# Performance work log

Hardware: AMD Instinct MI355X
Metric: run time of the kernel (lower is better)

The kernel has to match this reference:

```python
import jax, jax.numpy as jnp
import numpy as np

B, N, D_IN, D_OUT, L, T = 8, 512, 1024, 1024, 16, 4096


def setup_inputs() -> dict:
    key = jax.random.key(0)
    k1, k2, k3 = jax.random.split(key, 3)
    pooled_vectors = jax.random.normal(k1, (B, N, D_IN), dtype=jnp.float32)
    # stacked nn.Linear weights, each (out, in), bias=False
    W = jax.random.normal(k2, (L, D_OUT, D_IN), dtype=jnp.float32) * 0.02
    pooling_indices = jnp.sort(jax.random.randint(k3, (N,), 0, T, dtype=jnp.int64))
    return {
        "pooled_vectors": pooled_vectors,
        "W": W,
        "pooling_indices": pooling_indices,
        "target_length": T,
    }


def reference(pooled_vectors, W, pooling_indices, target_length):
    # pooled_vectors: (B, N, D_in); W: (L, D_out, D_in); pooling_indices: (N,) sorted
    Bn, Nn, _ = pooled_vectors.shape
    Ln = W.shape[0]
    t = jnp.arange(target_length)
    # segment i covers [start_i, idx_i + 1); searchsorted finds the covering segment
    seg = jnp.searchsorted(pooling_indices, t, side="left")  # (T,)
    valid = seg < Nn  # positions past the last pooling index stay zero
    segc = jnp.clip(seg, 0, Nn - 1)
    start = jnp.where(segc > 0, pooling_indices[segc - 1] + 1, 0)
    lidx = jnp.minimum(t - start, Ln - 1)  # position-specific linear index, capped
    # apply all L position linears to every pooled vector: (B, N, L, D_out)
    trans = jnp.einsum("bnd,lod->bnlo", pooled_vectors, W)
    out = trans[:, segc, lidx]  # gather per output position -> (B, T, D_out)
    return jnp.where(valid[None, :, None], out, jnp.zeros((), out.dtype))
```

## Files before the change

### kernel.cpp

```cpp
#include <hip/hip_runtime.h>
#include <stdint.h>

#define B_    8
#define N_    512
#define DIN   1024
#define DOUT  1024
#define L_    16
#define T_    4096

#define BM 256
#define BN 128
#define BK 32
#define NB (DOUT / BN)
#define NKT (DIN / BK)
#define MT_MAX 160
#define ZROW ((long)B_ * N_)

typedef __attribute__((ext_vector_type(8))) short short8;
typedef __attribute__((ext_vector_type(4))) float f32x4;

#define POOLED_ELEMS ((long)B_ * N_ * DIN + DIN)
#define WS_W_OFF     ((size_t)POOLED_ELEMS * 2)
#define WS_META_OFF  (WS_W_OFF + (size_t)L_ * DOUT * DIN * 2)

__device__ __forceinline__ unsigned short f2bf(float f) {
  unsigned u = __float_as_uint(f);
  u += 0x7FFFu + ((u >> 16) & 1u);
  return (unsigned short)(u >> 16);
}

__device__ __forceinline__ void gload_lds16(const void* g, void* l) {
  __builtin_amdgcn_global_load_lds(
      (const __attribute__((address_space(1))) void*)g,
      (__attribute__((address_space(3))) void*)l, 16, 0, 0);
}

__device__ __forceinline__ void bar() {
  asm volatile("" ::: "memory");
  __builtin_amdgcn_s_barrier();
  asm volatile("" ::: "memory");
}

__global__ void k_convert(const float* __restrict__ pooled,
                          const float* __restrict__ W,
                          unsigned short* __restrict__ wsP,
                          unsigned short* __restrict__ wsW) {
  const long np4 = (long)B_ * N_ * DIN / 4;
  const long nw4 = (long)L_ * DOUT * DIN / 4;
  const long nz4 = DIN / 4;
  long i = (long)blockIdx.x * blockDim.x + threadIdx.x;
  const long stride = (long)gridDim.x * blockDim.x;
  for (; i < np4 + nw4 + nz4; i += stride) {
    if (i < np4) {
      float4 v = ((const float4*)pooled)[i];
      ushort4 o = { f2bf(v.x), f2bf(v.y), f2bf(v.z), f2bf(v.w) };
      ((ushort4*)wsP)[i] = o;
    } else if (i < np4 + nw4) {
      float4 v = ((const float4*)W)[i - np4];
      ushort4 o = { f2bf(v.x), f2bf(v.y), f2bf(v.z), f2bf(v.w) };
      ((ushort4*)wsW)[i - np4] = o;
    } else {
      ushort4 z = {0, 0, 0, 0};
      ((ushort4*)wsP)[i - nw4] = z;
    }
  }
}

__global__ void k_prep(const int* __restrict__ pidx,
                       unsigned* __restrict__ tlist,
                       int* __restrict__ goff, int* __restrict__ grows,
                       unsigned* __restrict__ table, int* __restrict__ ntiles) {
  __shared__ int sp[N_];
  __shared__ unsigned smap[T_];
  __shared__ int cnt[L_], pos[L_];
  const int tid = threadIdx.x;
  for (int i = tid; i < N_; i += 256) sp[i] = pidx[i];
  if (tid < L_) cnt[tid] = 0;
  __syncthreads();
  for (int t = tid; t < T_; t += 256) {
    int lo = 0, hi = N_;
    while (lo < hi) { int mid = (lo + hi) >> 1; if (sp[mid] < t) lo = mid + 1; else hi = mid; }
    int n, l;
    if (lo < N_) {
      int start = lo ? sp[lo - 1] + 1 : 0;
      int li = t - start;
      l = li > (L_ - 1) ? (L_ - 1) : li;
      n = lo;
    } else { n = 0xFFFF; l = L_ - 1; }
    smap[t] = (unsigned)n | ((unsigned)l << 16);
    atomicAdd(&cnt[l], 1);
  }
  __syncthreads();
  if (tid == 0) {
    int off = 0;
    for (int l = 0; l < L_; ++l) {
      pos[l] = off; goff[l] = off; grows[l] = cnt[l] * B_;
      off += cnt[l];
    }
  }
  __syncthreads();
  for (int t = tid; t < T_; t += 256) {
    unsigned m = smap[t];
    int l = m >> 16;
    int p = atomicAdd(&pos[l], 1);
    tlist[p] = (unsigned)t | ((m & 0xFFFFu) << 16);
  }
  __syncthreads();
  if (tid == 0) {
    int tt = 0;
    for (int l = 0; l < L_; ++l) {
      int rows = cnt[l] * B_;
      for (int r0 = 0; r0 < rows; r0 += BM) table[tt++] = (unsigned)l | ((unsigned)r0 << 4);
    }
    *ntiles = tt;
  }
}

__global__ __launch_bounds__(512, 4)
void k_gemm(const unsigned short* __restrict__ wsP,
            const unsigned short* __restrict__ wsW,
            const unsigned* __restrict__ tlist,
            const int* __restrict__ goff,
            const int* __restrict__ grows,
            const unsigned* __restrict__ table,
            const int* __restrict__ ntiles,
            float* __restrict__ out) {
  const int bid = blockIdx.x;
  const int mt = bid >> 3;
  const int nt = bid & 7;
  if (mt >= *ntiles) return;

  const unsigned te = table[mt];
  const int l    = te & 15;
  const int row0 = (int)(te >> 4);
  const int toff = goff[l];
  const int rows = grows[l];

  __shared__ __align__(16) unsigned short As[3][BM * BK];
  __shared__ __align__(16) unsigned short Bs[3][BN * BK];

  const int tid  = threadIdx.x;
  const int lane = tid & 63;
  const int w    = tid >> 6;
  const int wm   = w >> 1;
  const int wn   = w & 1;

  const int srow = tid >> 2;
  const int sx4  = ((tid & 3) ^ (srow & 3)) * 16;
  const char* aptr0;
  const char* aptr1;
  {
    long re[2];
#pragma unroll
    for (int r = 0; r < 2; ++r) {
      int rg = row0 + r * 128 + srow;
      if (rg < rows) {
        unsigned e = tlist[toff + (rg >> 3)];
        unsigned n = e >> 16;
        int b = rg & 7;
        re[r] = (n == 0xFFFFu) ? ZROW * (long)DIN
                               : ((long)(b * N_ + (int)n)) * DIN;
      } else re[r] = ZROW * (long)DIN;
    }
    aptr0 = (const char*)(wsP + re[0]) + sx4;
    aptr1 = (const char*)(wsP + re[1]) + sx4;
  }
  const char* bptr = (const char*)(wsW + ((long)l * DOUT + nt * BN + srow) * DIN) + sx4;

#define STG(t_, sb) do { \
  gload_lds16(aptr0 + (t_) * 64, (char*)As[sb] + w * 1024); \
  gload_lds16(aptr1 + (t_) * 64, (char*)As[sb] + 8192 + w * 1024); \
  gload_lds16(bptr  + (t_) * 64, (char*)Bs[sb] + w * 1024); } while (0)

  const int arow = wm * 64 + (lane & 15);
  const int brow = wn * 64 + (lane & 15);
  const int axr  = ((lane >> 4) ^ (lane & 3)) * 16;

  f32x4 acc[4][4];
#pragma unroll
  for (int m = 0; m < 4; ++m)
#pragma unroll
    for (int n = 0; n < 4; ++n)
      acc[m][n] = (f32x4){0.f, 0.f, 0.f, 0.f};

  short8 af[4], bf[4];

#define PHASE(t_, bb, sb) do { \
  const int t2_ = (t_) + 2; \
  if (t2_ < NKT) STG(t2_, sb); \
  _Pragma("unroll") for (int m_ = 0; m_ < 4; ++m_) \
    af[m_] = *(const short8*)((const char*)As[bb] + (arow + m_ * 16) * 64 + axr); \
  _Pragma("unroll") for (int n_ = 0; n_ < 4; ++n_) \
    bf[n_] = *(const short8*)((const char*)Bs[bb] + (brow + n_ * 16) * 64 + axr); \
  bar(); \
  asm volatile("s_waitcnt lgkmcnt(0)" ::: "memory"); \
  __builtin_amdgcn_s_setprio(1); \
  _Pragma("unroll") for (int n_ = 0; n_ < 4; ++n_) \
    _Pragma("unroll") for (int m_ = 0; m_ < 4; ++m_) \
      acc[m_][n_] = __builtin_amdgcn_mfma_f32_16x16x32_bf16(af[m_], bf[n_], acc[m_][n_], 0, 0, 0); \
  __builtin_amdgcn_s_setprio(0); \
  if (t2_ < NKT) asm volatile("s_waitcnt vmcnt(3)" ::: "memory"); \
  else           asm volatile("s_waitcnt vmcnt(0)" ::: "memory"); \
  bar(); \
} while (0)

  STG(0, 0);
  STG(1, 1);
  asm volatile("s_waitcnt vmcnt(3)" ::: "memory");
  bar();

  for (int j = 0; j < 11; ++j) {
    const int t0 = 3 * j;
    if (t0     < NKT) PHASE(t0,     0, 2);
    if (t0 + 1 < NKT) PHASE(t0 + 1, 1, 0);
    if (t0 + 2 < NKT) PHASE(t0 + 2, 2, 1);
  }

#pragma unroll
  for (int m = 0; m < 4; ++m) {
#pragma unroll
    for (int jj = 0; jj < 4; ++jj) {
      int rt = wm * 64 + m * 16 + (lane >> 4) * 4 + jj;
      int rg = row0 + rt;
      if (rg >= rows) continue;
      unsigned e = tlist[toff + (rg >> 3)];
      int b = rg & 7;
      int tt = (int)(e & 0xFFFFu);
      float* orow = out + ((long)b * T_ + tt) * DOUT + nt * BN + wn * 64 + (lane & 15);
#pragma unroll
      for (int n = 0; n < 4; ++n)
        orow[n * 16] = acc[m][n][jj];
    }
  }
#undef STG
#undef PHASE
}

extern "C" void kernel_launch(void* const* d_in, const int* in_sizes, int n_in,
                              void* d_out, int out_size, void* d_ws, size_t ws_size,
                              hipStream_t stream) {
  const float* pooled = (const float*)d_in[0];
  const float* W      = (const float*)d_in[1];
  const int*   pidx   = (const int*)d_in[2];
  float* out = (float*)d_out;

  char* ws = (char*)d_ws;
  unsigned short* wsP = (unsigned short*)(ws);
  unsigned short* wsW = (unsigned short*)(ws + WS_W_OFF);
  int* meta  = (int*)(ws + WS_META_OFF);
  unsigned* tlist = (unsigned*)meta;
  int* goff  = meta + T_;
  int* grows = meta + T_ + 16;
  unsigned* table = (unsigned*)(meta + T_ + 32);
  int* ntiles = meta + T_ + 32 + MT_MAX;

  k_prep<<<1, 256, 0, stream>>>(pidx, tlist, goff, grows, table, ntiles);
  k_convert<<<2048, 256, 0, stream>>>(pooled, W, wsP, wsW);
  k_gemm<<<MT_MAX * NB, 512, 0, stream>>>(wsP, wsW, tlist, goff, grows, table,
                                          ntiles, out);
}
```

Measured before the change: 141.8 us.

## Deduplicate capped-index output rows and change LDS swizzle pattern

The prep kernel now walks segments instead of positions. All positions within a segment that share the capped linear index L-1, and all positions past the last pooling index, are merged into one GEMM row carrying a repeat count of up to 255. The GEMM epilogue writes each result row to consecutive output positions. This cuts the number of GEMM rows in the last group (and the zero rows) at the cost of a serial store loop in the epilogue. The LDS XOR swizzle also changes to use bits 1-2 of the row, meant to reduce bank conflicts.

```diff
diff --git a/kernel.cpp b/kernel.cpp
--- a/kernel.cpp
+++ b/kernel.cpp
@@ -71,46 +71,62 @@
                        int* __restrict__ goff, int* __restrict__ grows,
                        unsigned* __restrict__ table, int* __restrict__ ntiles) {
   __shared__ int sp[N_];
-  __shared__ unsigned smap[T_];
   __shared__ int cnt[L_], pos[L_];
   const int tid = threadIdx.x;
-  for (int i = tid; i < N_; i += 256) sp[i] = pidx[i];
+  if (tid < N_) sp[tid] = pidx[tid];
   if (tid < L_) cnt[tid] = 0;
   __syncthreads();
-  for (int t = tid; t < T_; t += 256) {
-    int lo = 0, hi = N_;
-    while (lo < hi) { int mid = (lo + hi) >> 1; if (sp[mid] < t) lo = mid + 1; else hi = mid; }
-    int n, l;
-    if (lo < N_) {
-      int start = lo ? sp[lo - 1] + 1 : 0;
-      int li = t - start;
-      l = li > (L_ - 1) ? (L_ - 1) : li;
-      n = lo;
-    } else { n = 0xFFFF; l = L_ - 1; }
-    smap[t] = (unsigned)n | ((unsigned)l << 16);
-    atomicAdd(&cnt[l], 1);
+
+  int start = tid ? sp[tid - 1] + 1 : 0;
+  int len = sp[tid] - start + 1;
+  if (len < 0) len = 0;
+  const int nfull = len < 15 ? len : 15;
+
+  for (int l2 = 0; l2 < nfull; ++l2) atomicAdd(&cnt[l2], 1);
+  if (len > 15) atomicAdd(&cnt[15], (len - 15 + 254) / 255);
+  if (tid == N_ - 1) {
+    int invlen = T_ - 1 - sp[N_ - 1];
+    if (invlen > 0) atomicAdd(&cnt[15], (invlen + 254) / 255);
   }
   __syncthreads();
   if (tid == 0) {
     int off = 0;
-    for (int l = 0; l < L_; ++l) {
-      pos[l] = off; goff[l] = off; grows[l] = cnt[l] * B_;
-      off += cnt[l];
-    }
-  }
-  __syncthreads();
-  for (int t = tid; t < T_; t += 256) {
-    unsigned m = smap[t];
-    int l = m >> 16;
-    int p = atomicAdd(&pos[l], 1);
-    tlist[p] = (unsigned)t | ((m & 0xFFFFu) << 16);
+    for (int l2 = 0; l2 < L_; ++l2) {
+      pos[l2] = off; goff[l2] = off; grows[l2] = cnt[l2] * B_;
+      off += cnt[l2];
+    }
+  }
+  __syncthreads();
+
+  for (int l2 = 0; l2 < nfull; ++l2) {
+    int p = atomicAdd(&pos[l2], 1);
+    tlist[p] = (unsigned)(start + l2) | ((unsigned)tid << 12) | (1u << 22);
+  }
+  if (len > 15) {
+    int rem = len - 15, tt2 = start + 15;
+    while (rem > 0) {
+      int rr = rem > 255 ? 255 : rem;
+      int p = atomicAdd(&pos[15], 1);
+      tlist[p] = (unsigned)tt2 | ((unsigned)tid << 12) | ((unsigned)rr << 22);
+      tt2 += rr; rem -= rr;
+    }
+  }
+  if (tid == N_ - 1) {
+    int tt2 = sp[N_ - 1] + 1;
+    int rem = T_ - tt2;
+    while (rem > 0) {
+      int rr = rem > 255 ? 255 : rem;
+      int p = atomicAdd(&pos[15], 1);
+      tlist[p] = (unsigned)tt2 | (1023u << 12) | ((unsigned)rr << 22);
+      tt2 += rr; rem -= rr;
+    }
   }
   __syncthreads();
   if (tid == 0) {
     int tt = 0;
-    for (int l = 0; l < L_; ++l) {
-      int rows = cnt[l] * B_;
-      for (int r0 = 0; r0 < rows; r0 += BM) table[tt++] = (unsigned)l | ((unsigned)r0 << 4);
+    for (int l2 = 0; l2 < L_; ++l2) {
+      int rows = cnt[l2] * B_;
+      for (int r0 = 0; r0 < rows; r0 += BM) table[tt++] = (unsigned)l2 | ((unsigned)r0 << 4);
     }
     *ntiles = tt;
   }
@@ -146,7 +162,7 @@
   const int wn   = w & 1;
 
   const int srow = tid >> 2;
-  const int sx4  = ((tid & 3) ^ (srow & 3)) * 16;
+  const int sx4  = ((tid & 3) ^ ((srow >> 1) & 3)) * 16;
   const char* aptr0;
   const char* aptr1;
   {
@@ -156,10 +172,10 @@
       int rg = row0 + r * 128 + srow;
       if (rg < rows) {
         unsigned e = tlist[toff + (rg >> 3)];
-        unsigned n = e >> 16;
+        unsigned n = (e >> 12) & 0x3FF;
         int b = rg & 7;
-        re[r] = (n == 0xFFFFu) ? ZROW * (long)DIN
-                               : ((long)(b * N_ + (int)n)) * DIN;
+        re[r] = (n >= N_) ? ZROW * (long)DIN
+                          : ((long)(b * N_ + (int)n)) * DIN;
       } else re[r] = ZROW * (long)DIN;
     }
     aptr0 = (const char*)(wsP + re[0]) + sx4;
@@ -174,7 +190,7 @@
 
   const int arow = wm * 64 + (lane & 15);
   const int brow = wn * 64 + (lane & 15);
-  const int axr  = ((lane >> 4) ^ (lane & 3)) * 16;
+  const int axr  = ((lane >> 4) ^ (((lane & 15) >> 1) & 3)) * 16;
 
   f32x4 acc[4][4];
 #pragma unroll
@@ -225,11 +241,15 @@
       if (rg >= rows) continue;
       unsigned e = tlist[toff + (rg >> 3)];
       int b = rg & 7;
-      int tt = (int)(e & 0xFFFFu);
-      float* orow = out + ((long)b * T_ + tt) * DOUT + nt * BN + wn * 64 + (lane & 15);
-#pragma unroll
-      for (int n = 0; n < 4; ++n)
-        orow[n * 16] = acc[m][n][jj];
+      int t0 = (int)(e & 0xFFFu);
+      int rep = (int)(e >> 22);
+      float* orow = out + ((long)b * T_ + t0) * DOUT + nt * BN + wn * 64 + (lane & 15);
+      for (int r = 0; r < rep; ++r) {
+#pragma unroll
+        for (int n = 0; n < 4; ++n)
+          orow[n * 16] = acc[m][n][jj];
+        orow += DOUT;
+      }
     }
   }
 #undef STG
@@ -249,12 +269,12 @@
   unsigned short* wsW = (unsigned short*)(ws + WS_W_OFF);
   int* meta  = (int*)(ws + WS_META_OFF);
   unsigned* tlist = (unsigned*)meta;
-  int* goff  = meta + T_;
-  int* grows = meta + T_ + 16;
-  unsigned* table = (unsigned*)(meta + T_ + 32);
-  int* ntiles = meta + T_ + 32 + MT_MAX;
-
-  k_prep<<<1, 256, 0, stream>>>(pidx, tlist, goff, grows, table, ntiles);
+  int* goff  = meta + 8 * T_;
+  int* grows = meta + 8 * T_ + 16;
+  unsigned* table = (unsigned*)(meta + 8 * T_ + 32);
+  int* ntiles = meta + 8 * T_ + 32 + MT_MAX;
+
+  k_prep<<<1, 512, 0, stream>>>(pidx, tlist, goff, grows, table, ntiles);
   k_convert<<<2048, 256, 0, stream>>>(pooled, W, wsP, wsW);
   k_gemm<<<MT_MAX * NB, 512, 0, stream>>>(wsP, wsW, tlist, goff, grows, table,
                                           ntiles, out);
```

Result: faster. 137.8 us (-2.8%).
